# Kernel optimization log

Measured on AMD Instinct MI355X. Metric: run time of the kernel, lower is better.

The kernel has to match this reference:

```python
import jax, jax.numpy as jnp
import numpy as np


def _conv(x, w, pad):
    return jax.lax.conv_general_dilated(
        x, w, (1, 1), [(pad, pad), (pad, pad)],
        dimension_numbers=('NCHW', 'OIHW', 'NCHW'))


def _avgpool2(x):
    B, C, H, W = x.shape
    return x.reshape(B, C, H // 2, 2, W // 2, 2).mean(axis=(3, 5))


def setup_inputs() -> dict:
    key = jax.random.key(0)
    ks = jax.random.split(key, 10)
    B = 1024
    x = jax.random.uniform(ks[0], (B, 1, 28, 28), jnp.float32)
    # depthwise-separable conv params (in=1 -> depthwise is a plain 3x3 conv)
    dw_w = jax.random.normal(ks[1], (1, 1, 3, 3), jnp.float32) * 0.3
    pw_w = jax.random.normal(ks[2], (32, 1, 1, 1), jnp.float32) * 0.3
    pw_b = jax.random.normal(ks[3], (32,), jnp.float32) * 0.05
    # fixed 4-qubit entangling unitary (real orthogonal 16x16), stand-in for tq.RandomLayer(n_ops=8)
    U = jnp.asarray(np.linalg.qr(np.random.default_rng(0).standard_normal((16, 16)))[0],
                    jnp.float32)
    fus_w = jax.random.normal(ks[4], (128, 36, 3, 3), jnp.float32) * (1.0 / np.sqrt(36 * 9))
    fus_b = jax.random.normal(ks[5], (128,), jnp.float32) * 0.05
    F = 128 * 7 * 7
    cls_w = jax.random.normal(ks[6], (10, F), jnp.float32) * (1.0 / np.sqrt(F))
    cls_b = jax.random.normal(ks[7], (10,), jnp.float32) * 0.05
    reg_w = jax.random.normal(ks[8], (1, F), jnp.float32) * (1.0 / np.sqrt(F))
    reg_b = jax.random.normal(ks[9], (1,), jnp.float32) * 0.05
    return {'x': x, 'dw_w': dw_w, 'pw_w': pw_w, 'pw_b': pw_b, 'U': U,
            'fus_w': fus_w, 'fus_b': fus_b, 'cls_w': cls_w, 'cls_b': cls_b,
            'reg_w': reg_w, 'reg_b': reg_b}


def _quantum_patches(x, U):
    # x: (B,1,28,28) -> 14x14 grid of 2x2 patches, 4 RY angles per patch
    B = x.shape[0]
    p = x.reshape(B, 14, 2, 14, 2).transpose(0, 1, 3, 2, 4).reshape(B, 14, 14, 4)
    h = 0.5 * p
    a = jnp.stack([jnp.cos(h), jnp.sin(h)], axis=-1)       # (B,14,14,4,2)
    # RY-encoded product state |psi> = kron over 4 wires -> 16 real amplitudes
    amp = jnp.einsum('...i,...j,...k,...l->...ijkl',
                     a[..., 0, :], a[..., 1, :], a[..., 2, :], a[..., 3, :]
                     ).reshape(B, 14, 14, 16)
    state = amp @ U.T                                       # entangling layer
    probs = state * state
    idx = jnp.arange(16)
    # PauliZ expectation per wire; wire 0 is the most significant bit
    signs = 1.0 - 2.0 * (((idx[None, :] >> (3 - jnp.arange(4)[:, None])) & 1)
                         .astype(jnp.float32))              # (4,16)
    meas = probs @ signs.T                                  # (B,14,14,4)
    # replicate torch.cat(patches,dim=1).view(B,4,14,14): flat row-major then reshape
    return meas.reshape(B, 14 * 14 * 4).reshape(B, 4, 14, 14)


def reference(x, dw_w, pw_w, pw_b, U, fus_w, fus_b, cls_w, cls_b, reg_w, reg_b):
    B = x.shape[0]
    out_ds = _conv(_conv(x, dw_w, 1), pw_w, 0) + pw_b[None, :, None, None]  # (B,32,28,28)
    out_q = _quantum_patches(x, U)                                          # (B,4,14,14)
    out = jnp.concatenate([_avgpool2(out_ds), out_q], axis=1)               # (B,36,14,14)
    out = jax.nn.relu(_conv(out, fus_w, 1) + fus_b[None, :, None, None])    # (B,128,14,14)
    out = _avgpool2(out)                                                    # (B,128,7,7)
    flat = out.reshape(B, -1)
    logits = flat @ cls_w.T + cls_b
    aux = flat @ reg_w.T + reg_b
    return (logits, aux)
```

## Files before the change

kernel.cpp:

```cpp
#include <hip/hip_runtime.h>
#include <math.h>


typedef __bf16 bf16x8 __attribute__((ext_vector_type(8)));
typedef float  f32x16 __attribute__((ext_vector_type(16)));

union Pack8 { __bf16 h[8]; uint4 v; };

__global__ __launch_bounds__(256) void prep(
    const float* __restrict__ fus_w,
    const float* __restrict__ cls_w,
    const float* __restrict__ reg_w,
    __bf16* __restrict__ bfrag,
    float* __restrict__ clsTT)
{
    const int gid = blockIdx.x * 256 + threadIdx.x;
    if (gid < 55296) {
        const int j    = gid & 7;
        const int frag = gid >> 3;
        const int lane = frag & 63;
        const int rest = frag >> 6;
        const int m  = rest % 27;
        const int nt = rest / 27;
        const int t  = m / 3, ks = m - t * 3;
        const int n  = nt * 32 + (lane & 31);
        const int ic = ks * 16 + (lane >> 5) * 8 + j;
        const float v = (ic < 36) ? fus_w[n * 324 + ic * 9 + t] : 0.f;
        bfrag[gid] = (__bf16)v;
    } else if (gid < 55296 + 86016) {
        const int e   = gid - 55296;
        const int kk  = e % 12;
        const int r0  = e / 12;
        const int l31 = r0 & 31;
        const int r1  = r0 >> 5;
        const int hk  = r1 & 1;
        const int r2  = r1 >> 1;
        const int q   = r2 & 3;
        const int r3  = r2 >> 2;
        const int mt  = r3 % 7;
        const int nt  = r3 / 7;
        const int oc   = nt * 32 + l31;
        const int cell = mt * 8 + q * 2 + hk;
        float v = 0.f;
        if (cell < 49 && kk < 11) {
            const int f = oc * 49 + cell;
            v = (kk < 10) ? cls_w[kk * 6272 + f] : reg_w[f];
        }
        clsTT[e] = v;
    }
}

__device__ __forceinline__ void patch_work(
    const int tid, const float* __restrict__ xs, __bf16* __restrict__ actT,
    const float* __restrict__ dw_w, const float* __restrict__ pw_w,
    const float* __restrict__ pw_b, const float* __restrict__ U)
{
    if (tid >= 196) return;
    const int i = tid / 14, j = tid % 14;
    const int Y = 2 * i, X = 2 * j;

    float w9[9];
    #pragma unroll
    for (int t = 0; t < 9; ++t) w9[t] = dw_w[t];
    float dsum = 0.f;
    #pragma unroll
    for (int dy = 0; dy < 2; ++dy) {
        #pragma unroll
        for (int dx = 0; dx < 2; ++dx) {
            const int cy = Y + dy, cx = X + dx;
            #pragma unroll
            for (int ky = 0; ky < 3; ++ky) {
                const int yy = cy + ky - 1;
                if (yy < 0 || yy > 27) continue;
                #pragma unroll
                for (int kx = 0; kx < 3; ++kx) {
                    const int xx = cx + kx - 1;
                    if (xx < 0 || xx > 27) continue;
                    dsum += xs[yy * 28 + xx] * w9[ky * 3 + kx];
                }
            }
        }
    }
    const float dpool = 0.25f * dsum;

    const int sp_o = (i + 1) * 16 + (j + 1);
    #pragma unroll
    for (int c8 = 0; c8 < 4; ++c8) {
        Pack8 pk;
        #pragma unroll
        for (int e = 0; e < 8; ++e)
            pk.h[e] = (__bf16)(pw_w[c8 * 8 + e] * dpool + pw_b[c8 * 8 + e]);
        ((uint4*)actT)[sp_o * 7 + c8] = pk.v;
    }

    const float p0 = xs[Y * 28 + X],       p1 = xs[Y * 28 + X + 1];
    const float p2 = xs[(Y + 1) * 28 + X], p3 = xs[(Y + 1) * 28 + X + 1];
    float c0, s0, c1, s1, c2, s2, c3, s3;
    sincosf(0.5f * p0, &s0, &c0);
    sincosf(0.5f * p1, &s1, &c1);
    sincosf(0.5f * p2, &s2, &c2);
    sincosf(0.5f * p3, &s3, &c3);
    float a01[4] = {c0 * c1, c0 * s1, s0 * c1, s0 * s1};
    float a23[4] = {c2 * c3, c2 * s3, s2 * c3, s2 * s3};
    float amp[16];
    #pragma unroll
    for (int hi = 0; hi < 4; ++hi)
        #pragma unroll
        for (int lo = 0; lo < 4; ++lo)
            amp[hi * 4 + lo] = a01[hi] * a23[lo];

    float meas[4] = {0.f, 0.f, 0.f, 0.f};
    #pragma unroll
    for (int m = 0; m < 16; ++m) {
        float st = 0.f;
        #pragma unroll
        for (int n = 0; n < 16; ++n) st = fmaf(U[m * 16 + n], amp[n], st);
        const float pm = st * st;
        meas[0] += ((m >> 3) & 1) ? -pm : pm;
        meas[1] += ((m >> 2) & 1) ? -pm : pm;
        meas[2] += ((m >> 1) & 1) ? -pm : pm;
        meas[3] += (m & 1) ? -pm : pm;
    }
    const int fbase = i * 56 + j * 4;
    #pragma unroll
    for (int w = 0; w < 4; ++w) {
        const int f  = fbase + w;
        const int ch = f / 196;
        const int sp = f - ch * 196;
        const int r2 = sp / 14 + 1, c2i = sp % 14 + 1;
        const int sp2 = r2 * 16 + c2i;
        actT[sp2 * 56 + 32 + ch] = (__bf16)meas[w];
    }
}

__device__ __forceinline__ void conv_fold(
    const __bf16* __restrict__ actT, const bf16x8* __restrict__ bfr,
    const float4* __restrict__ cls4, const float fb_l,
    const int l31, const int hk, float* __restrict__ a11)
{
    for (int mt = 0; mt < 7; ++mt) {
        const int mp   = mt * 32 + l31;
        const int cell = mp >> 2;
        const int cc = (cell < 49) ? cell : 48;
        const int py = (cc * 9363) >> 16;
        const int px = cc - py * 7;
        const int yy = 2 * py + ((mp >> 1) & 1);
        const int xx = 2 * px + (mp & 1);
        const int rowbase = yy * 16 + xx;

        f32x16 acc = {0.f,0.f,0.f,0.f,0.f,0.f,0.f,0.f,
                      0.f,0.f,0.f,0.f,0.f,0.f,0.f,0.f};

        #pragma unroll
        for (int t = 0; t < 9; ++t) {
            const int ky = t / 3, kx = t - ky * 3;
            const int row = rowbase + ky * 16 + kx;
            const __bf16* rp = actT + row * 56 + hk * 8;
            #pragma unroll
            for (int ks = 0; ks < 3; ++ks) {
                const bf16x8 af = *(const bf16x8*)(rp + ks * 16);
                acc = __builtin_amdgcn_mfma_f32_32x32x16_bf16(af, bfr[t * 3 + ks],
                                                              acc, 0, 0, 0);
            }
        }

        const float4* cwm = cls4 + mt * 768;
        #pragma unroll
        for (int q = 0; q < 4; ++q) {
            float pv = 0.f;
            #pragma unroll
            for (int s = 0; s < 4; ++s) {
                const float v = acc[q * 4 + s] + fb_l;
                pv += (v > 0.f ? v : 0.f);
            }
            pv *= 0.25f;
            const float4 w0 = cwm[q * 192 + 0];
            const float4 w1 = cwm[q * 192 + 1];
            const float4 w2 = cwm[q * 192 + 2];
            a11[0]  = fmaf(pv, w0.x, a11[0]);
            a11[1]  = fmaf(pv, w0.y, a11[1]);
            a11[2]  = fmaf(pv, w0.z, a11[2]);
            a11[3]  = fmaf(pv, w0.w, a11[3]);
            a11[4]  = fmaf(pv, w1.x, a11[4]);
            a11[5]  = fmaf(pv, w1.y, a11[5]);
            a11[6]  = fmaf(pv, w1.z, a11[6]);
            a11[7]  = fmaf(pv, w1.w, a11[7]);
            a11[8]  = fmaf(pv, w2.x, a11[8]);
            a11[9]  = fmaf(pv, w2.y, a11[9]);
            a11[10] = fmaf(pv, w2.z, a11[10]);
        }
    }
}

__global__ __launch_bounds__(256, 2) void quanv_fused(
    const float* __restrict__ x,
    const float* __restrict__ dw_w,
    const float* __restrict__ pw_w,
    const float* __restrict__ pw_b,
    const float* __restrict__ U,
    const __bf16* __restrict__ bfrag,
    const float* __restrict__ fus_b,
    const float* __restrict__ clsTT,
    const float* __restrict__ cls_b,
    const float* __restrict__ reg_b,
    float* __restrict__ out,
    int B)
{
    __shared__ __align__(16) __bf16 actT[2][256 * 56];
    __shared__ float xs[2][784];
    __shared__ float red[2][48];

    const int b0  = blockIdx.x * 2;
    const int b1  = b0 + 1;
    const bool two = (b1 < B);
    const int tid = threadIdx.x;

    {
        uint4 z; z.x = 0; z.y = 0; z.z = 0; z.w = 0;
        uint4* a4 = (uint4*)&actT[0][0];
        for (int i = tid; i < 3584; i += 256) a4[i] = z;
        const float* xb = x + (size_t)b0 * 784;
        const int tot = two ? 1568 : 784;
        float* xf = &xs[0][0];
        for (int i = tid; i < tot; i += 256) xf[i] = xb[i];
    }

    const int lane = tid & 63, nt = tid >> 6;
    const int l31  = lane & 31, hk = lane >> 5;
    const float fb_l = fus_b[nt * 32 + l31];

    bf16x8 bfr[27];
    {
        const bf16x8* __restrict__ bp = ((const bf16x8*)bfrag) + (nt * 27 * 64 + lane);
        #pragma unroll
        for (int m = 0; m < 27; ++m) bfr[m] = bp[m * 64];
    }

    const float4* __restrict__ cls4 =
        ((const float4*)clsTT) + ((((nt * 7) * 4) * 2 + hk) * 32 + l31) * 3;

    __syncthreads();

    patch_work(tid, &xs[0][0], &actT[0][0], dw_w, pw_w, pw_b, U);
    __syncthreads();

    float a11_0[11];
    #pragma unroll
    for (int k = 0; k < 11; ++k) a11_0[k] = 0.f;
    if (two) patch_work(tid, &xs[1][0], &actT[1][0], dw_w, pw_w, pw_b, U);
    conv_fold(&actT[0][0], bfr, cls4, fb_l, l31, hk, a11_0);
    __syncthreads();

    float a11_1[11];
    #pragma unroll
    for (int k = 0; k < 11; ++k) a11_1[k] = 0.f;
    if (two) conv_fold(&actT[1][0], bfr, cls4, fb_l, l31, hk, a11_1);

    #pragma unroll
    for (int k = 0; k < 11; ++k) {
        float a = a11_0[k];
        float c = a11_1[k];
        #pragma unroll
        for (int off = 32; off > 0; off >>= 1) {
            a += __shfl_down(a, off, 64);
            c += __shfl_down(c, off, 64);
        }
        if (lane == 0) { red[0][k * 4 + nt] = a; red[1][k * 4 + nt] = c; }
    }
    __syncthreads();
    if (tid < 11) {
        const float v = red[0][tid * 4] + red[0][tid * 4 + 1]
                      + red[0][tid * 4 + 2] + red[0][tid * 4 + 3];
        if (tid < 10) out[b0 * 10 + tid] = v + cls_b[tid];
        else          out[B * 10 + b0]   = v + reg_b[0];
    } else if (two && tid >= 64 && tid < 75) {
        const int k = tid - 64;
        const float v = red[1][k * 4] + red[1][k * 4 + 1]
                      + red[1][k * 4 + 2] + red[1][k * 4 + 3];
        if (k < 10) out[b1 * 10 + k] = v + cls_b[k];
        else        out[B * 10 + b1] = v + reg_b[0];
    }
}

extern "C" void kernel_launch(void* const* d_in, const int* in_sizes, int n_in,
                              void* d_out, int out_size, void* d_ws, size_t ws_size,
                              hipStream_t stream) {
    const float* x    = (const float*)d_in[0];
    const float* dw_w = (const float*)d_in[1];
    const float* pw_w = (const float*)d_in[2];
    const float* pw_b = (const float*)d_in[3];
    const float* U    = (const float*)d_in[4];
    const float* fw   = (const float*)d_in[5];
    const float* fb   = (const float*)d_in[6];
    const float* cw   = (const float*)d_in[7];
    const float* cb   = (const float*)d_in[8];
    const float* rw   = (const float*)d_in[9];
    const float* rb   = (const float*)d_in[10];
    const int B = in_sizes[0] / 784;

    __bf16* bfrag = (__bf16*)d_ws;
    float*  clsTT = (float*)((char*)d_ws + 110592);

    prep<<<(55296 + 86016 + 255) / 256, 256, 0, stream>>>(fw, cw, rw, bfrag, clsTT);
    const int nblk = (B + 1) / 2;
    quanv_fused<<<nblk, 256, 0, stream>>>(x, dw_w, pw_w, pw_b, U, bfrag, fb,
                                          clsTT, cb, rb, (float*)d_out, B);
}
```

Baseline: 110.6 us.

## Swizzle LDS activation layout and batch A-fragment loads with dual accumulators

The LDS activation tile row stride goes from 56 to 64 bf16, and the 16-byte chunks within each row are XOR-swizzled by spatial parity. The goal is to avoid LDS bank conflicts when lanes read neighbouring spatial positions for the MFMA A operands. The conv loop now loads all nine A fragments per kernel row before issuing its MFMAs, splits accumulation across two accumulator sets to shorten dependency chains, and raises wave priority around the MFMA bursts. The cost is more LDS (the zero-fill loop grows to match), more registers for the fragment buffer and second accumulator, and padded cells now map to different fallback positions.

```diff
diff --git a/kernel.cpp b/kernel.cpp
--- a/kernel.cpp
+++ b/kernel.cpp
@@ -6,6 +6,10 @@
 typedef float  f32x16 __attribute__((ext_vector_type(16)));
 
 union Pack8 { __bf16 h[8]; uint4 v; };
+
+__device__ __forceinline__ int swz_h(int Y, int X) {
+    return (X & 1) | ((Y & 1) << 1) | ((((Y >> 1) + (X >> 1)) & 1) << 2);
+}
 
 __global__ __launch_bounds__(256) void prep(
     const float* __restrict__ fus_w,
@@ -83,14 +87,16 @@
     }
     const float dpool = 0.25f * dsum;
 
-    const int sp_o = (i + 1) * 16 + (j + 1);
+    const int Yr = i + 1, Xr = j + 1;
+    const int sp_o = Yr * 16 + Xr;
+    const int hb = swz_h(Yr, Xr);
     #pragma unroll
     for (int c8 = 0; c8 < 4; ++c8) {
         Pack8 pk;
         #pragma unroll
         for (int e = 0; e < 8; ++e)
             pk.h[e] = (__bf16)(pw_w[c8 * 8 + e] * dpool + pw_b[c8 * 8 + e]);
-        ((uint4*)actT)[sp_o * 7 + c8] = pk.v;
+        ((uint4*)actT)[sp_o * 8 + (c8 ^ hb)] = pk.v;
     }
 
     const float p0 = xs[Y * 28 + X],       p1 = xs[Y * 28 + X + 1];
@@ -129,7 +135,8 @@
         const int sp = f - ch * 196;
         const int r2 = sp / 14 + 1, c2i = sp % 14 + 1;
         const int sp2 = r2 * 16 + c2i;
-        actT[sp2 * 56 + 32 + ch] = (__bf16)meas[w];
+        const int hb2 = swz_h(r2, c2i);
+        actT[sp2 * 64 + ((4 ^ hb2) << 3) + ch] = (__bf16)meas[w];
     }
 }
 
@@ -139,29 +146,51 @@
     const int l31, const int hk, float* __restrict__ a11)
 {
     for (int mt = 0; mt < 7; ++mt) {
-        const int mp   = mt * 32 + l31;
-        const int cell = mp >> 2;
-        const int cc = (cell < 49) ? cell : 48;
-        const int py = (cc * 9363) >> 16;
-        const int px = cc - py * 7;
-        const int yy = 2 * py + ((mp >> 1) & 1);
-        const int xx = 2 * px + (mp & 1);
-        const int rowbase = yy * 16 + xx;
-
-        f32x16 acc = {0.f,0.f,0.f,0.f,0.f,0.f,0.f,0.f,
-                      0.f,0.f,0.f,0.f,0.f,0.f,0.f,0.f};
-
-        #pragma unroll
-        for (int t = 0; t < 9; ++t) {
-            const int ky = t / 3, kx = t - ky * 3;
-            const int row = rowbase + ky * 16 + kx;
-            const __bf16* rp = actT + row * 56 + hk * 8;
+        const int slot = l31 >> 2;
+        int cell = mt * 8 + slot;
+        if (cell > 48) cell = (slot & 1);
+        const int py = (cell * 9363) >> 16;
+        const int px = cell - py * 7;
+        const int yy = 2 * py + ((l31 >> 1) & 1);
+        const int xx = 2 * px + (l31 & 1);
+
+        f32x16 acc0 = {0.f,0.f,0.f,0.f,0.f,0.f,0.f,0.f,
+                       0.f,0.f,0.f,0.f,0.f,0.f,0.f,0.f};
+        f32x16 acc1 = {0.f,0.f,0.f,0.f,0.f,0.f,0.f,0.f,
+                       0.f,0.f,0.f,0.f,0.f,0.f,0.f,0.f};
+
+        #pragma unroll
+        for (int ky = 0; ky < 3; ++ky) {
+            const int Yk = yy + ky;
+            bf16x8 af[9];
             #pragma unroll
-            for (int ks = 0; ks < 3; ++ks) {
-                const bf16x8 af = *(const bf16x8*)(rp + ks * 16);
-                acc = __builtin_amdgcn_mfma_f32_32x32x16_bf16(af, bfr[t * 3 + ks],
-                                                              acc, 0, 0, 0);
+            for (int kx = 0; kx < 3; ++kx) {
+                const int Xk = xx + kx;
+                const int r  = Yk * 16 + Xk;
+                const int hb = swz_h(Yk, Xk);
+                const __bf16* rp = actT + r * 64;
+                #pragma unroll
+                for (int ks = 0; ks < 3; ++ks)
+                    af[kx * 3 + ks] =
+                        *(const bf16x8*)(rp + (((2 * ks + hk) ^ hb) << 3));
             }
+            __builtin_amdgcn_s_setprio(1);
+            if (ky == 1) {
+                #pragma unroll
+                for (int kx = 0; kx < 3; ++kx)
+                    #pragma unroll
+                    for (int ks = 0; ks < 3; ++ks)
+                        acc1 = __builtin_amdgcn_mfma_f32_32x32x16_bf16(
+                            af[kx * 3 + ks], bfr[(ky * 3 + kx) * 3 + ks], acc1, 0, 0, 0);
+            } else {
+                #pragma unroll
+                for (int kx = 0; kx < 3; ++kx)
+                    #pragma unroll
+                    for (int ks = 0; ks < 3; ++ks)
+                        acc0 = __builtin_amdgcn_mfma_f32_32x32x16_bf16(
+                            af[kx * 3 + ks], bfr[(ky * 3 + kx) * 3 + ks], acc0, 0, 0, 0);
+            }
+            __builtin_amdgcn_s_setprio(0);
         }
 
         const float4* cwm = cls4 + mt * 768;
@@ -170,7 +199,7 @@
             float pv = 0.f;
             #pragma unroll
             for (int s = 0; s < 4; ++s) {
-                const float v = acc[q * 4 + s] + fb_l;
+                const float v = acc0[q * 4 + s] + acc1[q * 4 + s] + fb_l;
                 pv += (v > 0.f ? v : 0.f);
             }
             pv *= 0.25f;
@@ -206,7 +235,7 @@
     float* __restrict__ out,
     int B)
 {
-    __shared__ __align__(16) __bf16 actT[2][256 * 56];
+    __shared__ __align__(16) __bf16 actT[2][256 * 64];
     __shared__ float xs[2][784];
     __shared__ float red[2][48];
 
@@ -218,7 +247,7 @@
     {
         uint4 z; z.x = 0; z.y = 0; z.z = 0; z.w = 0;
         uint4* a4 = (uint4*)&actT[0][0];
-        for (int i = tid; i < 3584; i += 256) a4[i] = z;
+        for (int i = tid; i < 4096; i += 256) a4[i] = z;
         const float* xb = x + (size_t)b0 * 784;
         const int tot = two ? 1568 : 784;
         float* xf = &xs[0][0];
```

Result: slower. 116.1 us (+4.9%).

## Pack quantum channels across conv taps to cut zero-padded MFMA work

Applied to the files above, without the earlier changes.

Splits the fused 3x3 conv's K dimension so the 32 depthwise channels use 2 MFMA k-steps per tap and the 4 quantum channels are packed four taps per MFMA in a separate LDS buffer. This cuts MFMAs per tile from 27 to 21 and removes the padding from 36 to 48 channels. It also shrinks the activation LDS stride and B-fragment registers. In exchange it adds extra small 8-byte LDS gathers with per-lane tap offsets and changes the weight prep layout.

```diff
diff --git a/kernel.cpp b/kernel.cpp
--- a/kernel.cpp
+++ b/kernel.cpp
@@ -3,9 +3,11 @@
 
 
 typedef __bf16 bf16x8 __attribute__((ext_vector_type(8)));
+typedef __bf16 bf16x4 __attribute__((ext_vector_type(4)));
 typedef float  f32x16 __attribute__((ext_vector_type(16)));
 
 union Pack8 { __bf16 h[8]; uint4 v; };
+union QPair { struct { bf16x4 lo, hi; } p; bf16x8 v; };
 
 __global__ __launch_bounds__(256) void prep(
     const float* __restrict__ fus_w,
@@ -15,20 +17,30 @@
     float* __restrict__ clsTT)
 {
     const int gid = blockIdx.x * 256 + threadIdx.x;
-    if (gid < 55296) {
+    if (gid < 43008) {
         const int j    = gid & 7;
         const int frag = gid >> 3;
         const int lane = frag & 63;
         const int rest = frag >> 6;
-        const int m  = rest % 27;
-        const int nt = rest / 27;
-        const int t  = m / 3, ks = m - t * 3;
+        const int m  = rest % 21;
+        const int nt = rest / 21;
         const int n  = nt * 32 + (lane & 31);
-        const int ic = ks * 16 + (lane >> 5) * 8 + j;
-        const float v = (ic < 36) ? fus_w[n * 324 + ic * 9 + t] : 0.f;
+        const int hk = lane >> 5;
+        float v;
+        if (m < 18) {
+            const int t = m >> 1, ks = m & 1;
+            const int ic = ks * 16 + hk * 8 + j;
+            v = fus_w[n * 324 + ic * 9 + t];
+        } else {
+            const int ps = m - 18;
+            const int k  = hk * 8 + j;
+            const int tap = ps * 4 + (k >> 2);
+            const int ch  = k & 3;
+            v = (tap < 9) ? fus_w[n * 324 + (32 + ch) * 9 + tap] : 0.f;
+        }
         bfrag[gid] = (__bf16)v;
-    } else if (gid < 55296 + 86016) {
-        const int e   = gid - 55296;
+    } else if (gid < 43008 + 86016) {
+        const int e   = gid - 43008;
         const int kk  = e % 12;
         const int r0  = e / 12;
         const int l31 = r0 & 31;
@@ -52,6 +64,7 @@
 
 __device__ __forceinline__ void patch_work(
     const int tid, const float* __restrict__ xs, __bf16* __restrict__ actT,
+    __bf16* __restrict__ Qt,
     const float* __restrict__ dw_w, const float* __restrict__ pw_w,
     const float* __restrict__ pw_b, const float* __restrict__ U)
 {
@@ -90,7 +103,7 @@
         #pragma unroll
         for (int e = 0; e < 8; ++e)
             pk.h[e] = (__bf16)(pw_w[c8 * 8 + e] * dpool + pw_b[c8 * 8 + e]);
-        ((uint4*)actT)[sp_o * 7 + c8] = pk.v;
+        ((uint4*)actT)[sp_o * 5 + c8] = pk.v;
     }
 
     const float p0 = xs[Y * 28 + X],       p1 = xs[Y * 28 + X + 1];
@@ -129,14 +142,16 @@
         const int sp = f - ch * 196;
         const int r2 = sp / 14 + 1, c2i = sp % 14 + 1;
         const int sp2 = r2 * 16 + c2i;
-        actT[sp2 * 56 + 32 + ch] = (__bf16)meas[w];
+        Qt[sp2 * 4 + ch] = (__bf16)meas[w];
     }
 }
 
 __device__ __forceinline__ void conv_fold(
-    const __bf16* __restrict__ actT, const bf16x8* __restrict__ bfr,
-    const float4* __restrict__ cls4, const float fb_l,
-    const int l31, const int hk, float* __restrict__ a11)
+    const __bf16* __restrict__ actT, const __bf16* __restrict__ Qt,
+    const bf16x8* __restrict__ bfr, const float4* __restrict__ cls4,
+    const float fb_l, const int l31, const int hk,
+    const int* __restrict__ offL, const int* __restrict__ offH,
+    float* __restrict__ a11)
 {
     for (int mt = 0; mt < 7; ++mt) {
         const int mp   = mt * 32 + l31;
@@ -155,13 +170,21 @@
         for (int t = 0; t < 9; ++t) {
             const int ky = t / 3, kx = t - ky * 3;
             const int row = rowbase + ky * 16 + kx;
-            const __bf16* rp = actT + row * 56 + hk * 8;
+            const __bf16* rp = actT + row * 40 + hk * 8;
             #pragma unroll
-            for (int ks = 0; ks < 3; ++ks) {
+            for (int ks = 0; ks < 2; ++ks) {
                 const bf16x8 af = *(const bf16x8*)(rp + ks * 16);
-                acc = __builtin_amdgcn_mfma_f32_32x32x16_bf16(af, bfr[t * 3 + ks],
+                acc = __builtin_amdgcn_mfma_f32_32x32x16_bf16(af, bfr[t * 2 + ks],
                                                               acc, 0, 0, 0);
             }
+        }
+        #pragma unroll
+        for (int ps = 0; ps < 3; ++ps) {
+            QPair u;
+            u.p.lo = *(const bf16x4*)(Qt + (rowbase + offL[ps]) * 4);
+            u.p.hi = *(const bf16x4*)(Qt + (rowbase + offH[ps]) * 4);
+            acc = __builtin_amdgcn_mfma_f32_32x32x16_bf16(u.v, bfr[18 + ps],
+                                                          acc, 0, 0, 0);
         }
 
         const float4* cwm = cls4 + mt * 768;
@@ -206,7 +229,8 @@
     float* __restrict__ out,
     int B)
 {
-    __shared__ __align__(16) __bf16 actT[2][256 * 56];
+    __shared__ __align__(16) __bf16 actT[2][256 * 40];
+    __shared__ __align__(16) __bf16 Qt[2][256 * 4];
     __shared__ float xs[2][784];
     __shared__ float red[2][48];
 
@@ -218,7 +242,9 @@
     {
         uint4 z; z.x = 0; z.y = 0; z.z = 0; z.w = 0;
         uint4* a4 = (uint4*)&actT[0][0];
-        for (int i = tid; i < 3584; i += 256) a4[i] = z;
+        for (int i = tid; i < 2560; i += 256) a4[i] = z;
+        uint4* q4 = (uint4*)&Qt[0][0];
+        for (int i = tid; i < 256; i += 256) q4[i] = z;
         const float* xb = x + (size_t)b0 * 784;
         const int tot = two ? 1568 : 784;
         float* xf = &xs[0][0];
@@ -229,11 +255,22 @@
     const int l31  = lane & 31, hk = lane >> 5;
     const float fb_l = fus_b[nt * 32 + l31];
 
-    bf16x8 bfr[27];
+    bf16x8 bfr[21];
     {
-        const bf16x8* __restrict__ bp = ((const bf16x8*)bfrag) + (nt * 27 * 64 + lane);
-        #pragma unroll
-        for (int m = 0; m < 27; ++m) bfr[m] = bp[m * 64];
+        const bf16x8* __restrict__ bp = ((const bf16x8*)bfrag) + (nt * 21 * 64 + lane);
+        #pragma unroll
+        for (int m = 0; m < 21; ++m) bfr[m] = bp[m * 64];
+    }
+
+    int offL[3], offH[3];
+    #pragma unroll
+    for (int ps = 0; ps < 3; ++ps) {
+        int tL = ps * 4 + hk * 2;
+        int tH = tL + 1;
+        if (tL > 8) tL = 0;
+        if (tH > 8) tH = 0;
+        offL[ps] = (tL / 3) * 16 + (tL % 3);
+        offH[ps] = (tH / 3) * 16 + (tH % 3);
     }
 
     const float4* __restrict__ cls4 =
@@ -241,20 +278,20 @@
 
     __syncthreads();
 
-    patch_work(tid, &xs[0][0], &actT[0][0], dw_w, pw_w, pw_b, U);
+    patch_work(tid, &xs[0][0], &actT[0][0], &Qt[0][0], dw_w, pw_w, pw_b, U);
     __syncthreads();
 
     float a11_0[11];
     #pragma unroll
     for (int k = 0; k < 11; ++k) a11_0[k] = 0.f;
-    if (two) patch_work(tid, &xs[1][0], &actT[1][0], dw_w, pw_w, pw_b, U);
-    conv_fold(&actT[0][0], bfr, cls4, fb_l, l31, hk, a11_0);
+    if (two) patch_work(tid, &xs[1][0], &actT[1][0], &Qt[1][0], dw_w, pw_w, pw_b, U);
+    conv_fold(&actT[0][0], &Qt[0][0], bfr, cls4, fb_l, l31, hk, offL, offH, a11_0);
     __syncthreads();
 
     float a11_1[11];
     #pragma unroll
     for (int k = 0; k < 11; ++k) a11_1[k] = 0.f;
-    if (two) conv_fold(&actT[1][0], bfr, cls4, fb_l, l31, hk, a11_1);
+    if (two) conv_fold(&actT[1][0], &Qt[1][0], bfr, cls4, fb_l, l31, hk, offL, offH, a11_1);
 
     #pragma unroll
     for (int k = 0; k < 11; ++k) {
@@ -299,9 +336,9 @@
     const int B = in_sizes[0] / 784;
 
     __bf16* bfrag = (__bf16*)d_ws;
-    float*  clsTT = (float*)((char*)d_ws + 110592);
-
-    prep<<<(55296 + 86016 + 255) / 256, 256, 0, stream>>>(fw, cw, rw, bfrag, clsTT);
+    float*  clsTT = (float*)((char*)d_ws + 86016);
+
+    prep<<<(43008 + 86016 + 255) / 256, 256, 0, stream>>>(fw, cw, rw, bfrag, clsTT);
     const int nblk = (B + 1) / 2;
     quanv_fused<<<nblk, 256, 0, stream>>>(x, dw_w, pw_w, pw_b, U, bfrag, fb,
                                           clsTT, cb, rb, (float*)d_out, B);
```

After: 108.2 us. 1.02x faster.
